# Kernel optimization log

Measured on AMD Instinct MI355X. Metric: run time of the kernel, lower is better.

Reference implementation:

```python
import jax, jax.numpy as jnp
import numpy as np

B, R, D = 16, 2048, 512
H2, NREL = 2 * D, 2048  # relation_mlp hidden = 2*d_model, output = n_relations
MIN_PROB = 0.1          # early-stop probability threshold from the torch code


def setup_inputs() -> dict:
    key = jax.random.key(0)
    ks = jax.random.split(key, 8)
    sc = lambda k, shp: jax.random.normal(k, shp, jnp.float32) * 0.02
    return {
        "rel_encoding": jax.random.normal(ks[0], (B, R, D), jnp.float32),
        "na_emb": jax.random.normal(ks[1], (D,), jnp.float32),
        "v_w": sc(ks[2], (D, D)), "v_b": jnp.zeros((D,), jnp.float32),
        "o_w": sc(ks[3], (D, D)), "o_b": jnp.zeros((D,), jnp.float32),
        "ln_g": jnp.ones((D,), jnp.float32), "ln_b": jnp.zeros((D,), jnp.float32),
        "w1": sc(ks[4], (H2, D)), "b1": jnp.zeros((H2,), jnp.float32),
        "w2": sc(ks[5], (NREL, H2)), "b2": jnp.zeros((NREL,), jnp.float32),
    }


def _ln(x, g, b, eps=1e-5):
    m = jnp.mean(x, axis=-1, keepdims=True)
    v = jnp.var(x, axis=-1, keepdims=True)
    return (x - m) * jax.lax.rsqrt(v + eps) * g + b


def reference(rel_encoding, na_emb, v_w, v_b, o_w, o_b, ln_g, ln_b, w1, b1, w2, b2):
    # Cross-attention with a single key/value token: softmax over a length-1 axis
    # is identically 1, so attn_out = out_proj(v_proj(kv)) for every query position.
    x = rel_encoding                                         # [B,R,D]
    attn = (x @ v_w.T + v_b) @ o_w.T + o_b                   # [B,R,D]

    def step_logits(state):                                  # state broadcasts to [B,R,D]
        h = _ln(attn + state, ln_g, ln_b)                    # residual + layernorm
        return jax.nn.relu(h @ w1.T + b1) @ w2.T + b2        # [B,R,NREL]

    # step 0: query is the na_embedding
    p0 = jax.nn.softmax(step_logits(na_emb), axis=-1)
    m0 = jnp.max(p0, axis=-1)
    i0 = jnp.argmax(p0, axis=-1)
    cont0 = (i0 != 0) & (m0 >= MIN_PROB)                     # else break before step 0 emits

    # step 1: last appended state is the relation encoding itself
    p1 = jax.nn.softmax(step_logits(x), axis=-1)
    m1 = jnp.max(p1, axis=-1)
    i1 = jnp.argmax(p1, axis=-1)
    cont1 = cont0 & (i1 != 0) & (m1 >= MIN_PROB)

    # rule_score = prod of accepted step probs; 0.0 if no step accepted
    scores = jnp.where(cont0, jnp.where(cont1, m0 * m1, m0), 0.0)  # [B,R]
    lengths = cont0.astype(jnp.int32) + cont1.astype(jnp.int32)    # ragged rule lengths
    return scores, i0, i1, lengths
```

## Files before the change

kernel.cpp:

```cpp
#include <hip/hip_runtime.h>
#include <math.h>

#define MTOT 32768
#define DD   512
#define HHD  1024
#define NRELN 2048
#define SCA  64.f
#define SCB  1024.f
#define INVS (1.f / 65536.f)
#define CAPR 4096
#define MARGIN 2.0e-3f

typedef _Float16 h8  __attribute__((ext_vector_type(8)));
typedef float    f16v __attribute__((ext_vector_type(16)));

__device__ __forceinline__ void fsplit(float x, _Float16& h, _Float16& l) {
  _Float16 t = (_Float16)x;
  h = t;
  l = (_Float16)(x - (float)t);
}

__device__ __forceinline__ void gld16(const _Float16* g, _Float16* l) {
  __builtin_amdgcn_global_load_lds(
      (const __attribute__((address_space(1))) void*)g,
      (__attribute__((address_space(3))) void*)l, 16, 0, 0);
}


__global__ void prep_wvo_split(const float* __restrict__ vw, const float* __restrict__ ow,
                               _Float16* __restrict__ wh, _Float16* __restrict__ wl) {
  int idx = blockIdx.x * 256 + threadIdx.x;
  int k = idx & 511;
  int n = idx >> 9;
  float s = 0.f;
  for (int j = 0; j < DD; ++j) s += ow[n * DD + j] * vw[j * DD + k];
  fsplit(s * SCB, wh[n * DD + k], wl[n * DD + k]);
}

__global__ void prep_cvec(const float* __restrict__ ow, const float* __restrict__ vb,
                          const float* __restrict__ ob, float* __restrict__ c) {
  int i = blockIdx.x * 256 + threadIdx.x;
  if (i < DD) {
    float s = ob[i];
    for (int k = 0; k < DD; ++k) s += ow[i * DD + k] * vb[k];
    c[i] = s;
  }
}

__global__ void prep_w1p_split(const float* __restrict__ w1, const float* __restrict__ g,
                               _Float16* __restrict__ wh, _Float16* __restrict__ wl) {
  int idx = blockIdx.x * 256 + threadIdx.x;
  int k = idx & 511;
  int n = idx >> 9;
  fsplit(w1[n * DD + k] * g[k] * SCB, wh[n * DD + k], wl[n * DD + k]);
}

__global__ void prep_b1p(const float* __restrict__ w1, const float* __restrict__ lnb,
                         const float* __restrict__ b1, float* __restrict__ b1p) {
  int n = blockIdx.x * 256 + threadIdx.x;
  if (n < HHD) {
    float s = b1[n];
    for (int k = 0; k < DD; ++k) s += w1[n * DD + k] * lnb[k];
    b1p[n] = s;
  }
}

__global__ void prep_w2_split(const float* __restrict__ w2,
                              _Float16* __restrict__ wh, _Float16* __restrict__ wl) {
  int idx = blockIdx.x * 256 + threadIdx.x;
  int k = idx & 1023;
  int n = idx >> 10;
  fsplit(w2[n * HHD + k] * SCB, wh[n * HHD + k], wl[n * HHD + k]);
}

__global__ void split_x(const float* __restrict__ src, _Float16* __restrict__ h,
                        _Float16* __restrict__ l) {
  int idx = (blockIdx.x * 256 + threadIdx.x) * 8;
  float4 a = *(const float4*)(src + idx);
  float4 b = *(const float4*)(src + idx + 4);
  float vv[8] = {a.x, a.y, a.z, a.w, b.x, b.y, b.z, b.w};
  _Float16 hh[8], ll[8];
#pragma unroll
  for (int i = 0; i < 8; ++i) fsplit(vv[i] * SCA, hh[i], ll[i]);
  *(h8*)(h + idx) = *(h8*)hh;
  *(h8*)(l + idx) = *(h8*)ll;
}

__global__ void zero_cnt(int* c) { c[blockIdx.x * 256 + threadIdx.x] = 0; }

template <int MODE, int KDIM, int NTOT>
__global__ __launch_bounds__(256) void gemm_split(
    const _Float16* __restrict__ Ah, const _Float16* __restrict__ Al,
    const _Float16* __restrict__ Bh, const _Float16* __restrict__ Bl,
    const float* __restrict__ bias,
    float* __restrict__ outF,
    _Float16* __restrict__ outHh, _Float16* __restrict__ outHl,
    float* __restrict__ pM, float* __restrict__ pI,
    const int* __restrict__ cntp, int pstr) {
  __shared__ __align__(16) _Float16 sA[2][128][32];
  __shared__ __align__(16) _Float16 sB[2][128][32];
  const int t = threadIdx.x;
  const int lane = t & 63;
  const int wv = t >> 6;
  const int wr = wv & 1, wc = wv >> 1;
  const int l31 = lane & 31, half = lane >> 5;
  const int n0 = blockIdx.y << 7;

  const _Float16* gsp = (wv == 0) ? Ah : (wv == 1) ? Al : (wv == 2) ? Bh : Bl;
  _Float16* lbase = (wv == 0) ? &sA[0][0][0] : (wv == 1) ? &sA[1][0][0]
                  : (wv == 2) ? &sB[0][0][0] : &sB[1][0][0];
  const int srow = lane >> 2;
  const int scp = lane & 3;
  const int swzE = ((srow >> 1) & 3) ^ ((srow >> 3) & 1);
  const int swzO = swzE ^ 2;
  const int swz = ((l31 >> 1) ^ (l31 >> 3)) & 3;

  int nmb;
  if constexpr (MODE == 2) {
    int a = *cntp;
    if (a > CAPR) a = CAPR;
    nmb = (a + 127) >> 7;
  } else {
    nmb = gridDim.x;
  }

  for (int mb = blockIdx.x; mb < nmb; mb += gridDim.x) {
    const int m0 = mb << 7;
    const int gb = (wv < 2) ? m0 : n0;
    const _Float16* gA0 = gsp + (size_t)(gb + srow) * KDIM + ((scp ^ swzE) << 3);
    const _Float16* gA1 = gsp + (size_t)(gb + srow) * KDIM + ((scp ^ swzO) << 3);

    f16v acc[2][2] = {};
    for (int k0 = 0; k0 < KDIM; k0 += 32) {
      __syncthreads();
#pragma unroll
      for (int it = 0; it < 8; ++it)
        gld16(((it & 1) ? gA1 : gA0) + (size_t)(it * 16) * KDIM + k0, lbase + it * 512);
      __syncthreads();
#pragma unroll
      for (int ks = 0; ks < 2; ++ks) {
        const int pos = (((ks << 1) + half) ^ swz) << 3;
        h8 af_h[2], af_l[2], bf_h[2], bf_l[2];
#pragma unroll
        for (int i = 0; i < 2; ++i) {
          const int mr = wr * 64 + i * 32 + l31;
          af_h[i] = *(const h8*)&sA[0][mr][pos];
          af_l[i] = *(const h8*)&sA[1][mr][pos];
        }
#pragma unroll
        for (int j = 0; j < 2; ++j) {
          const int nr = wc * 64 + j * 32 + l31;
          bf_h[j] = *(const h8*)&sB[0][nr][pos];
          bf_l[j] = *(const h8*)&sB[1][nr][pos];
        }
#pragma unroll
        for (int j = 0; j < 2; ++j)
#pragma unroll
          for (int i = 0; i < 2; ++i) {
            acc[i][j] = __builtin_amdgcn_mfma_f32_32x32x16_f16(af_h[i], bf_h[j], acc[i][j], 0, 0, 0);
            acc[i][j] = __builtin_amdgcn_mfma_f32_32x32x16_f16(af_h[i], bf_l[j], acc[i][j], 0, 0, 0);
            acc[i][j] = __builtin_amdgcn_mfma_f32_32x32x16_f16(af_l[i], bf_h[j], acc[i][j], 0, 0, 0);
          }
      }
    }

    float bb[2];
    int gc[2];
#pragma unroll
    for (int j = 0; j < 2; ++j) {
      gc[j] = n0 + wc * 64 + j * 32 + l31;
      bb[j] = bias[gc[j]];
    }
    if constexpr (MODE == 0) {
#pragma unroll
      for (int i = 0; i < 2; ++i)
#pragma unroll
        for (int r = 0; r < 16; ++r) {
          const int row = m0 + wr * 64 + i * 32 + (r & 3) + 8 * (r >> 2) + 4 * half;
#pragma unroll
          for (int j = 0; j < 2; ++j)
            outF[(size_t)row * NTOT + gc[j]] = acc[i][j][r] * INVS + bb[j];
        }
    } else if constexpr (MODE == 1) {
#pragma unroll
      for (int i = 0; i < 2; ++i)
#pragma unroll
        for (int r = 0; r < 16; ++r) {
          const int row = m0 + wr * 64 + i * 32 + (r & 3) + 8 * (r >> 2) + 4 * half;
#pragma unroll
          for (int j = 0; j < 2; ++j) {
            float v = fmaxf(acc[i][j][r] * INVS + bb[j], 0.f) * SCA;
            _Float16 hh, ll;
            fsplit(v, hh, ll);
            outHh[(size_t)row * NTOT + gc[j]] = hh;
            outHl[(size_t)row * NTOT + gc[j]] = ll;
          }
        }
    } else {
      const int slot = blockIdx.y * 2 + wc;
#pragma unroll
      for (int i = 0; i < 2; ++i)
#pragma unroll
        for (int r = 0; r < 16; ++r) {
          float v0 = acc[i][0][r] * INVS + bb[0];
          float v1 = acc[i][1][r] * INVS + bb[1];
          float M;
          int I;
          if (v0 >= v1) { M = v0; I = gc[0]; }
          else          { M = v1; I = gc[1]; }
#pragma unroll
          for (int sh = 1; sh <= 16; sh <<= 1) {
            float M2 = __shfl_xor(M, sh);
            int   I2 = __shfl_xor(I, sh);
            if (M2 > M || (M2 == M && I2 < I)) { M = M2; I = I2; }
          }
          if (l31 == 0) {
            const int grow = m0 + wr * 64 + i * 32 + (r & 3) + 8 * (r >> 2) + 4 * half;
            pM[(size_t)slot * pstr + grow] = M;
            pI[(size_t)slot * pstr + grow] = (float)I;
          }
        }
    }
  }
}

__global__ __launch_bounds__(256) void gemm_approx(
    const _Float16* __restrict__ Ah, const _Float16* __restrict__ Bh,
    const float* __restrict__ bias,
    float* __restrict__ pM, float* __restrict__ pM2,
    float* __restrict__ pS, int* __restrict__ pI, int astr) {
  __shared__ __align__(16) _Float16 sAB[12288];
  const int t = threadIdx.x;
  const int lane = t & 63;
  const int wv = t >> 6;
  const int wr = wv & 1, wc = wv >> 1;
  const int l31 = lane & 31, half = lane >> 5;
  const int m0 = blockIdx.x << 7;
  const int n0 = blockIdx.y << 8;

  const _Float16* gsrc[6];
  _Float16* ldst[6];
#pragma unroll
  for (int it = 0; it < 6; ++it) {
    int p = (it * 4 + wv) * 64 + lane;
    const _Float16* s;
    if (p < 512) {
      int row = p >> 2, cp = p & 3;
      int sw = ((row >> 1) ^ (row >> 3)) & 3;
      s = Ah + (size_t)(m0 + row) * HHD + ((cp ^ sw) << 3);
    } else {
      int pq = p - 512;
      int row = pq >> 2, cp = pq & 3;
      int sw = ((row >> 1) ^ (row >> 3)) & 3;
      s = Bh + (size_t)(n0 + row) * HHD + ((cp ^ sw) << 3);
    }
    gsrc[it] = s;
    ldst[it] = sAB + (size_t)(it * 4 + wv) * 512;
  }
  const int swz = ((l31 >> 1) ^ (l31 >> 3)) & 3;

  f16v acc[2][4] = {};
  for (int k0 = 0; k0 < HHD; k0 += 32) {
    __syncthreads();
#pragma unroll
    for (int it = 0; it < 6; ++it) gld16(gsrc[it] + k0, ldst[it]);
    __syncthreads();
#pragma unroll
    for (int ks = 0; ks < 2; ++ks) {
      const int pos = (((ks << 1) + half) ^ swz) << 3;
      h8 af[2], bf[4];
#pragma unroll
      for (int i = 0; i < 2; ++i)
        af[i] = *(const h8*)&sAB[(size_t)(wr * 64 + i * 32 + l31) * 32 + pos];
#pragma unroll
      for (int j = 0; j < 4; ++j)
        bf[j] = *(const h8*)&sAB[4096 + (size_t)(wc * 128 + j * 32 + l31) * 32 + pos];
#pragma unroll
      for (int j = 0; j < 4; ++j)
#pragma unroll
        for (int i = 0; i < 2; ++i)
          acc[i][j] = __builtin_amdgcn_mfma_f32_32x32x16_f16(af[i], bf[j], acc[i][j], 0, 0, 0);
    }
  }

  const int slot = blockIdx.y * 2 + wc;
  float bb[4];
  int gc[4];
#pragma unroll
  for (int j = 0; j < 4; ++j) {
    gc[j] = n0 + wc * 128 + j * 32 + l31;
    bb[j] = bias[gc[j]];
  }
#pragma unroll
  for (int i = 0; i < 2; ++i)
#pragma unroll
    for (int r = 0; r < 16; ++r) {
      float M = acc[i][0][r] * INVS + bb[0], M2 = -INFINITY, S = 1.f;
      int I = gc[0];
#pragma unroll
      for (int j = 1; j < 4; ++j) {
        float v = acc[i][j][r] * INVS + bb[j];
        if (v > M || (v == M && gc[j] < I)) {
          S = S * __expf(M - v) + 1.f; M2 = M; M = v; I = gc[j];
        } else {
          S += __expf(v - M); M2 = fmaxf(M2, v);
        }
      }
#pragma unroll
      for (int sh = 1; sh <= 16; sh <<= 1) {
        float Mo = __shfl_xor(M, sh);
        float M2o = __shfl_xor(M2, sh);
        float So = __shfl_xor(S, sh);
        int   Io = __shfl_xor(I, sh);
        if (Mo > M || (Mo == M && Io < I)) {
          S = S * __expf(M - Mo) + So; M2 = fmaxf(M, M2o); M = Mo; I = Io;
        } else {
          S += So * __expf(Mo - M); M2 = fmaxf(M2, Mo);
        }
      }
      if (l31 == 0) {
        const int grow = m0 + wr * 64 + i * 32 + (r & 3) + 8 * (r >> 2) + 4 * half;
        pM[(size_t)slot * astr + grow] = M;
        pM2[(size_t)slot * astr + grow] = M2;
        pS[(size_t)slot * astr + grow] = S;
        pI[(size_t)slot * astr + grow] = I;
      }
    }
}

__global__ void flag_k(const float* __restrict__ pM, const float* __restrict__ pM2,
                       const float* __restrict__ pS, const int* __restrict__ pI,
                       int astr, int rows,
                       float* __restrict__ map, int* __restrict__ iap, int row0,
                       int* __restrict__ list, int* __restrict__ cnt) {
  int r = blockIdx.x * 256 + threadIdx.x;
  if (r >= rows) return;
  float M = pM[r], M2 = pM2[r], S = pS[r];
  int I = pI[r];
  for (int s = 1; s < 16; ++s) {
    size_t o = (size_t)s * astr + r;
    float m = pM[o], m2 = pM2[o], ss = pS[o];
    int ii = pI[o];
    if (m > M || (m == M && ii < I)) {
      M2 = fmaxf(M, m2); S = S * __expf(M - m) + ss; M = m; I = ii;
    } else {
      M2 = fmaxf(M2, m); S += ss * __expf(m - M);
    }
  }
  map[row0 + r] = 1.f / S;
  iap[row0 + r] = I;
  if (M - M2 < MARGIN) {
    int c = atomicAdd(cnt, 1);
    if (c < CAPR) list[c] = r;
  }
}

__global__ void gather_k(const _Float16* __restrict__ Hh, const _Float16* __restrict__ Hl,
                         const int* __restrict__ list, const int* __restrict__ cnt,
                         _Float16* __restrict__ Gh, _Float16* __restrict__ Gl) {
  int b = blockIdx.x;
  int active = *cnt;
  if (active > CAPR) active = CAPR;
  if (b >= active) return;
  int r = list[b];
  int t = threadIdx.x;
  *(h8*)(Gh + (size_t)b * HHD + t * 8) = *(const h8*)(Hh + (size_t)r * HHD + t * 8);
  *(h8*)(Gl + (size_t)b * HHD + t * 8) = *(const h8*)(Hl + (size_t)r * HHD + t * 8);
}

__global__ void rescue_merge(const float* __restrict__ pMr, const float* __restrict__ pIr,
                             const int* __restrict__ list, const int* __restrict__ cnt,
                             int* __restrict__ iap, int row0) {
  int c = blockIdx.x * 256 + threadIdx.x;
  int a = *cnt;
  if (a > CAPR) a = CAPR;
  if (c >= a) return;
  float M = pMr[c];
  int I = (int)pIr[c];
  for (int s = 1; s < 32; ++s) {
    size_t o = (size_t)s * CAPR + c;
    float m = pMr[o];
    int i2 = (int)pIr[o];
    if (m > M || (m == M && i2 < I)) { M = m; I = i2; }
  }
  iap[row0 + list[c]] = I;
}

__global__ __launch_bounds__(256) void ln_dual(
    const float* __restrict__ A, const float* __restrict__ X,
    const float* __restrict__ na,
    _Float16* __restrict__ y0h, _Float16* __restrict__ y0l,
    _Float16* __restrict__ y1h, _Float16* __restrict__ y1l) {
  int t = threadIdx.x;
  int lane = t & 63;
  int w = t >> 6;
  int r = blockIdx.x * 4 + w;
  const float* ap = A + (size_t)r * DD + lane * 8;
  const float* xp = X + (size_t)r * DD + lane * 8;
  const float* np = na + lane * 8;
  float v0[8], v1[8];
  float s0 = 0.f, q0 = 0.f, s1 = 0.f, q1 = 0.f;
#pragma unroll
  for (int i = 0; i < 8; ++i) {
    float a = ap[i];
    v0[i] = a + np[i];
    v1[i] = a + xp[i];
    s0 += v0[i]; q0 += v0[i] * v0[i];
    s1 += v1[i]; q1 += v1[i] * v1[i];
  }
#pragma unroll
  for (int m = 1; m <= 32; m <<= 1) {
    s0 += __shfl_xor(s0, m); q0 += __shfl_xor(q0, m);
    s1 += __shfl_xor(s1, m); q1 += __shfl_xor(q1, m);
  }
  float mu0 = s0 * (1.f / DD), mu1 = s1 * (1.f / DD);
  float rs0 = 1.f / sqrtf(q0 * (1.f / DD) - mu0 * mu0 + 1e-5f);
  float rs1 = 1.f / sqrtf(q1 * (1.f / DD) - mu1 * mu1 + 1e-5f);
  _Float16 h0[8], l0[8], h1[8], l1[8];
#pragma unroll
  for (int i = 0; i < 8; ++i) {
    fsplit((v0[i] - mu0) * rs0 * SCA, h0[i], l0[i]);
    fsplit((v1[i] - mu1) * rs1 * SCA, h1[i], l1[i]);
  }
  *(h8*)(y0h + (size_t)r * DD + lane * 8) = *(h8*)h0;
  *(h8*)(y0l + (size_t)r * DD + lane * 8) = *(h8*)l0;
  *(h8*)(y1h + (size_t)r * DD + lane * 8) = *(h8*)h1;
  *(h8*)(y1l + (size_t)r * DD + lane * 8) = *(h8*)l1;
}

__global__ void finalize_k(const float* __restrict__ map0, const int* __restrict__ iap0,
                           const float* __restrict__ map1, const int* __restrict__ iap1,
                           float* __restrict__ out) {
  int r = blockIdx.x * 256 + threadIdx.x;
  float m0v = map0[r], m1v = map1[r];
  int i0v = iap0[r], i1v = iap1[r];
  bool c0 = (i0v != 0) && (m0v >= 0.1f);
  bool c1 = c0 && (i1v != 0) && (m1v >= 0.1f);
  out[r] = c0 ? (c1 ? m0v * m1v : m0v) : 0.f;
  out[MTOT + r] = (float)i0v;
  out[2 * MTOT + r] = (float)i1v;
  out[3 * MTOT + r] = (float)((c0 ? 1 : 0) + (c1 ? 1 : 0));
}

extern "C" void kernel_launch(void* const* d_in, const int* in_sizes, int n_in,
                              void* d_out, int out_size, void* d_ws, size_t ws_size,
                              hipStream_t stream) {
  const float* X   = (const float*)d_in[0];
  const float* na  = (const float*)d_in[1];
  const float* vw  = (const float*)d_in[2];
  const float* vb  = (const float*)d_in[3];
  const float* ow  = (const float*)d_in[4];
  const float* ob  = (const float*)d_in[5];
  const float* lng = (const float*)d_in[6];
  const float* lnb = (const float*)d_in[7];
  const float* w1  = (const float*)d_in[8];
  const float* b1  = (const float*)d_in[9];
  const float* w2  = (const float*)d_in[10];
  const float* b2  = (const float*)d_in[11];
  float* out = (float*)d_out;

  char* p = (char*)d_ws;
  auto alloc = [&](size_t bytes) -> void* {
    void* r = (void*)p;
    p += (bytes + 255) & ~(size_t)255;
    return r;
  };
  _Float16* wvo_h = (_Float16*)alloc(512 * 512 * 2);
  _Float16* wvo_l = (_Float16*)alloc(512 * 512 * 2);
  float*    cvec  = (float*)alloc(512 * 4);
  _Float16* w1p_h = (_Float16*)alloc(1024 * 512 * 2);
  _Float16* w1p_l = (_Float16*)alloc(1024 * 512 * 2);
  float*    b1p   = (float*)alloc(1024 * 4);
  _Float16* w2_h  = (_Float16*)alloc(2048 * 1024 * 2);
  _Float16* w2_l  = (_Float16*)alloc(2048 * 1024 * 2);
  float* map0 = (float*)alloc((size_t)MTOT * 4);
  float* map1 = (float*)alloc((size_t)MTOT * 4);
  int* iap0 = (int*)alloc((size_t)MTOT * 4);
  int* iap1 = (int*)alloc((size_t)MTOT * 4);
  int* list = (int*)alloc(CAPR * 4);
  int* cnt  = (int*)alloc(512 * 4);
  float* pMr = (float*)alloc((size_t)32 * CAPR * 4);
  float* pIr = (float*)alloc((size_t)32 * CAPR * 4);
  _Float16* Gh = (_Float16*)alloc((size_t)CAPR * HHD * 2);
  _Float16* Gl = (_Float16*)alloc((size_t)CAPR * HHD * 2);

  size_t fixed = (size_t)(p - (char*)d_ws);
  size_t reserve = 2u << 20;
  size_t remain = ws_size > fixed + reserve ? ws_size - fixed - reserve : 0;
  int chunk = (int)(remain / 10496);
  chunk &= ~127;
  if (chunk < 128) chunk = 128;
  if (chunk > MTOT) chunk = MTOT;

  _Float16* xs_h = (_Float16*)alloc((size_t)chunk * 512 * 2);
  _Float16* xs_l = (_Float16*)alloc((size_t)chunk * 512 * 2);
  float*    Abuf = (float*)alloc((size_t)chunk * 512 * 4);
  _Float16* y0_h = (_Float16*)alloc((size_t)chunk * 512 * 2);
  _Float16* y0_l = (_Float16*)alloc((size_t)chunk * 512 * 2);
  _Float16* H_h  = (_Float16*)alloc((size_t)chunk * 1024 * 2);
  _Float16* H_l  = (_Float16*)alloc((size_t)chunk * 1024 * 2);
  float* pMa  = (float*)alloc((size_t)16 * chunk * 4);
  float* pM2a = (float*)alloc((size_t)16 * chunk * 4);
  float* pSa  = (float*)alloc((size_t)16 * chunk * 4);
  int*   pIa  = (int*)alloc((size_t)16 * chunk * 4);
  _Float16* y1_h = xs_h;
  _Float16* y1_l = xs_l;

  zero_cnt<<<2, 256, 0, stream>>>(cnt);
  prep_wvo_split<<<1024, 256, 0, stream>>>(vw, ow, wvo_h, wvo_l);
  prep_cvec<<<2, 256, 0, stream>>>(ow, vb, ob, cvec);
  prep_w1p_split<<<2048, 256, 0, stream>>>(w1, lng, w1p_h, w1p_l);
  prep_b1p<<<4, 256, 0, stream>>>(w1, lnb, b1, b1p);
  prep_w2_split<<<8192, 256, 0, stream>>>(w2, w2_h, w2_l);

  int citer = 0;
  for (int row0 = 0; row0 < MTOT; row0 += chunk, ++citer) {
    int rows = (MTOT - row0 < chunk) ? (MTOT - row0) : chunk;
    split_x<<<rows * 512 / 2048, 256, 0, stream>>>(X + (size_t)row0 * 512, xs_h, xs_l);
    gemm_split<0, 512, 512><<<dim3(rows / 128, 4), 256, 0, stream>>>(
        xs_h, xs_l, wvo_h, wvo_l, cvec, Abuf, nullptr, nullptr,
        nullptr, nullptr, nullptr, 0);
    ln_dual<<<rows / 4, 256, 0, stream>>>(Abuf, X + (size_t)row0 * 512, na,
                                          y0_h, y0_l, y1_h, y1_l);
    for (int s = 0; s < 2; ++s) {
      int* cp = cnt + citer * 2 + s;
      gemm_split<1, 512, 1024><<<dim3(rows / 128, 8), 256, 0, stream>>>(
          s == 0 ? y0_h : y1_h, s == 0 ? y0_l : y1_l, w1p_h, w1p_l, b1p,
          nullptr, H_h, H_l, nullptr, nullptr, nullptr, 0);
      gemm_approx<<<dim3(rows / 128, 8), 256, 0, stream>>>(
          H_h, w2_h, b2, pMa, pM2a, pSa, pIa, chunk);
      flag_k<<<(rows + 255) / 256, 256, 0, stream>>>(
          pMa, pM2a, pSa, pIa, chunk, rows,
          s == 0 ? map0 : map1, s == 0 ? iap0 : iap1, row0, list, cp);
      gather_k<<<CAPR, 128, 0, stream>>>(H_h, H_l, list, cp, Gh, Gl);
      gemm_split<2, 1024, 2048><<<dim3(8, 16), 256, 0, stream>>>(
          Gh, Gl, w2_h, w2_l, b2, nullptr, nullptr, nullptr,
          pMr, pIr, cp, CAPR);
      rescue_merge<<<CAPR / 256, 256, 0, stream>>>(
          pMr, pIr, list, cp, s == 0 ? iap0 : iap1, row0);
    }
  }
  finalize_k<<<MTOT / 256, 256, 0, stream>>>(map0, iap0, map1, iap1, out);
}
```

Baseline: 1.635 ms.

## Retile approximate logit GEMM to 128x128 blocks with 16x16x32 MFMA

The approximate second-layer GEMM drops from 128x256 to 128x128 output tiles and switches from 32x32x16 to 16x16x32 MFMA instructions. Each wave now owns a 64x64 subtile with 4x4 accumulators. The partial softmax stats are written to 32 column slots instead of 16, so flag_k merges more partials and the workspace per row grows. The aim is more blocks in flight, less LDS per block and a cheaper shuffle reduction, at the cost of lower operand reuse per block and extra partial traffic.

Measured after the change: 1.591 ms. -2.7%, faster.

```diff
diff --git a/kernel.cpp b/kernel.cpp
--- a/kernel.cpp
+++ b/kernel.cpp
@@ -12,6 +12,7 @@
 #define MARGIN 2.0e-3f
 
 typedef _Float16 h8  __attribute__((ext_vector_type(8)));
+typedef float    f4  __attribute__((ext_vector_type(4)));
 typedef float    f16v __attribute__((ext_vector_type(16)));
 
 __device__ __forceinline__ void fsplit(float x, _Float16& h, _Float16& l) {
@@ -229,58 +230,56 @@
     const float* __restrict__ bias,
     float* __restrict__ pM, float* __restrict__ pM2,
     float* __restrict__ pS, int* __restrict__ pI, int astr) {
-  __shared__ __align__(16) _Float16 sAB[12288];
+  __shared__ __align__(16) _Float16 sAll[8192];
   const int t = threadIdx.x;
   const int lane = t & 63;
   const int wv = t >> 6;
   const int wr = wv & 1, wc = wv >> 1;
-  const int l31 = lane & 31, half = lane >> 5;
+  const int q = lane >> 4, l16 = lane & 15;
   const int m0 = blockIdx.x << 7;
-  const int n0 = blockIdx.y << 8;
-
-  const _Float16* gsrc[6];
-  _Float16* ldst[6];
-#pragma unroll
-  for (int it = 0; it < 6; ++it) {
-    int p = (it * 4 + wv) * 64 + lane;
-    const _Float16* s;
-    if (p < 512) {
-      int row = p >> 2, cp = p & 3;
-      int sw = ((row >> 1) ^ (row >> 3)) & 3;
-      s = Ah + (size_t)(m0 + row) * HHD + ((cp ^ sw) << 3);
-    } else {
-      int pq = p - 512;
-      int row = pq >> 2, cp = pq & 3;
-      int sw = ((row >> 1) ^ (row >> 3)) & 3;
-      s = Bh + (size_t)(n0 + row) * HHD + ((cp ^ sw) << 3);
-    }
-    gsrc[it] = s;
-    ldst[it] = sAB + (size_t)(it * 4 + wv) * 512;
-  }
-  const int swz = ((l31 >> 1) ^ (l31 >> 3)) & 3;
-
-  f16v acc[2][4] = {};
+  const int n0 = blockIdx.y << 7;
+
+  const _Float16* src0[4];
+#pragma unroll
+  for (int it = 0; it < 4; ++it) {
+    int p = it * 256 + t;
+    int row = (p & 511) >> 2;
+    int cp = p & 3;
+    int sw = ((row >> 1) ^ (row >> 3)) & 3;
+    const _Float16* base = (p < 512) ? (Ah + (size_t)(m0 + row) * HHD)
+                                     : (Bh + (size_t)(n0 + row) * HHD);
+    src0[it] = base + ((cp ^ sw) << 3);
+  }
+  _Float16* dstw = sAll + (size_t)(wv * 64) * 8;
+
+  int offA[4], offB[4];
+#pragma unroll
+  for (int i = 0; i < 4; ++i) {
+    int ra = wr * 64 + i * 16 + l16;
+    int swa = ((ra >> 1) ^ (ra >> 3)) & 3;
+    offA[i] = ra * 32 + ((q ^ swa) << 3);
+    int rb = wc * 64 + i * 16 + l16;
+    int swb = ((rb >> 1) ^ (rb >> 3)) & 3;
+    offB[i] = 4096 + rb * 32 + ((q ^ swb) << 3);
+  }
+
+  f4 acc[4][4] = {};
   for (int k0 = 0; k0 < HHD; k0 += 32) {
     __syncthreads();
 #pragma unroll
-    for (int it = 0; it < 6; ++it) gld16(gsrc[it] + k0, ldst[it]);
+    for (int it = 0; it < 4; ++it)
+      gld16(src0[it] + k0, dstw + it * 2048);
     __syncthreads();
-#pragma unroll
-    for (int ks = 0; ks < 2; ++ks) {
-      const int pos = (((ks << 1) + half) ^ swz) << 3;
-      h8 af[2], bf[4];
-#pragma unroll
-      for (int i = 0; i < 2; ++i)
-        af[i] = *(const h8*)&sAB[(size_t)(wr * 64 + i * 32 + l31) * 32 + pos];
-#pragma unroll
-      for (int j = 0; j < 4; ++j)
-        bf[j] = *(const h8*)&sAB[4096 + (size_t)(wc * 128 + j * 32 + l31) * 32 + pos];
-#pragma unroll
-      for (int j = 0; j < 4; ++j)
-#pragma unroll
-        for (int i = 0; i < 2; ++i)
-          acc[i][j] = __builtin_amdgcn_mfma_f32_32x32x16_f16(af[i], bf[j], acc[i][j], 0, 0, 0);
-    }
+    h8 af[4], bf[4];
+#pragma unroll
+    for (int i = 0; i < 4; ++i) af[i] = *(const h8*)&sAll[offA[i]];
+#pragma unroll
+    for (int j = 0; j < 4; ++j) bf[j] = *(const h8*)&sAll[offB[j]];
+#pragma unroll
+    for (int j = 0; j < 4; ++j)
+#pragma unroll
+      for (int i = 0; i < 4; ++i)
+        acc[i][j] = __builtin_amdgcn_mfma_f32_16x16x32_f16(af[i], bf[j], acc[i][j], 0, 0, 0);
   }
 
   const int slot = blockIdx.y * 2 + wc;
@@ -288,18 +287,18 @@
   int gc[4];
 #pragma unroll
   for (int j = 0; j < 4; ++j) {
-    gc[j] = n0 + wc * 128 + j * 32 + l31;
+    gc[j] = n0 + wc * 64 + j * 16 + l16;
     bb[j] = bias[gc[j]];
   }
 #pragma unroll
-  for (int i = 0; i < 2; ++i)
-#pragma unroll
-    for (int r = 0; r < 16; ++r) {
-      float M = acc[i][0][r] * INVS + bb[0], M2 = -INFINITY, S = 1.f;
+  for (int i = 0; i < 4; ++i)
+#pragma unroll
+    for (int rr = 0; rr < 4; ++rr) {
+      float M = acc[i][0][rr] * INVS + bb[0], M2 = -INFINITY, S = 1.f;
       int I = gc[0];
 #pragma unroll
       for (int j = 1; j < 4; ++j) {
-        float v = acc[i][j][r] * INVS + bb[j];
+        float v = acc[i][j][rr] * INVS + bb[j];
         if (v > M || (v == M && gc[j] < I)) {
           S = S * __expf(M - v) + 1.f; M2 = M; M = v; I = gc[j];
         } else {
@@ -307,7 +306,7 @@
         }
       }
 #pragma unroll
-      for (int sh = 1; sh <= 16; sh <<= 1) {
+      for (int sh = 1; sh <= 8; sh <<= 1) {
         float Mo = __shfl_xor(M, sh);
         float M2o = __shfl_xor(M2, sh);
         float So = __shfl_xor(S, sh);
@@ -318,8 +317,8 @@
           S += So * __expf(Mo - M); M2 = fmaxf(M2, Mo);
         }
       }
-      if (l31 == 0) {
-        const int grow = m0 + wr * 64 + i * 32 + (r & 3) + 8 * (r >> 2) + 4 * half;
+      if (l16 == 0) {
+        const int grow = m0 + wr * 64 + i * 16 + q * 4 + rr;
         pM[(size_t)slot * astr + grow] = M;
         pM2[(size_t)slot * astr + grow] = M2;
         pS[(size_t)slot * astr + grow] = S;
@@ -337,7 +336,7 @@
   if (r >= rows) return;
   float M = pM[r], M2 = pM2[r], S = pS[r];
   int I = pI[r];
-  for (int s = 1; s < 16; ++s) {
+  for (int s = 1; s < 32; ++s) {
     size_t o = (size_t)s * astr + r;
     float m = pM[o], m2 = pM2[o], ss = pS[o];
     int ii = pI[o];
@@ -487,7 +486,7 @@
   size_t fixed = (size_t)(p - (char*)d_ws);
   size_t reserve = 2u << 20;
   size_t remain = ws_size > fixed + reserve ? ws_size - fixed - reserve : 0;
-  int chunk = (int)(remain / 10496);
+  int chunk = (int)(remain / 10752);
   chunk &= ~127;
   if (chunk < 128) chunk = 128;
   if (chunk > MTOT) chunk = MTOT;
@@ -499,10 +498,10 @@
   _Float16* y0_l = (_Float16*)alloc((size_t)chunk * 512 * 2);
   _Float16* H_h  = (_Float16*)alloc((size_t)chunk * 1024 * 2);
   _Float16* H_l  = (_Float16*)alloc((size_t)chunk * 1024 * 2);
-  float* pMa  = (float*)alloc((size_t)16 * chunk * 4);
-  float* pM2a = (float*)alloc((size_t)16 * chunk * 4);
-  float* pSa  = (float*)alloc((size_t)16 * chunk * 4);
-  int*   pIa  = (int*)alloc((size_t)16 * chunk * 4);
+  float* pMa  = (float*)alloc((size_t)32 * chunk * 4);
+  float* pM2a = (float*)alloc((size_t)32 * chunk * 4);
+  float* pSa  = (float*)alloc((size_t)32 * chunk * 4);
+  int*   pIa  = (int*)alloc((size_t)32 * chunk * 4);
   _Float16* y1_h = xs_h;
   _Float16* y1_l = xs_l;
 
@@ -527,7 +526,7 @@
       gemm_split<1, 512, 1024><<<dim3(rows / 128, 8), 256, 0, stream>>>(
           s == 0 ? y0_h : y1_h, s == 0 ? y0_l : y1_l, w1p_h, w1p_l, b1p,
           nullptr, H_h, H_l, nullptr, nullptr, nullptr, 0);
-      gemm_approx<<<dim3(rows / 128, 8), 256, 0, stream>>>(
+      gemm_approx<<<dim3(rows / 128, 16), 256, 0, stream>>>(
           H_h, w2_h, b2, pMa, pM2a, pSa, pIa, chunk);
       flag_k<<<(rows + 255) / 256, 256, 0, stream>>>(
           pMa, pM2a, pSa, pIa, chunk, rows,
```
